# Kernel tuning notes

Hardware: AMD Instinct MI355X
Metric: run time of the kernel (lower is better)

Reference implementation:

```python
import jax, jax.numpy as jnp
from jax import lax
import numpy as np

NPOINT, K, EPS = 2048, 16, 1e-5


def fps(xyz, npoint):
    # Farthest point sampling. Deterministic start index 0 (torch uses randint).
    B, N, _ = xyz.shape
    def step(carry, _):
        distance, far = carry
        centroid = jnp.take_along_axis(xyz, far[:, None, None], axis=1)  # [B,1,3]
        d = jnp.sum((xyz - centroid) ** 2, axis=-1)                      # [B,N]
        distance = jnp.minimum(distance, d)
        return (distance, jnp.argmax(distance, axis=-1)), far
    init = (jnp.full((B, N), 1e10, dtype=xyz.dtype), jnp.zeros((B,), jnp.int32))
    _, cent = lax.scan(step, init, None, length=npoint)  # [npoint, B]
    return jnp.transpose(cent)  # [B, npoint]


def gather(points, idx):
    # points [B,N,C], idx [B,...] -> [B,...,C]
    return jax.vmap(lambda p, i: p[i])(points, idx)


def bn_relu(x, gamma, beta):
    # x [B,S,K,C]; BatchNorm2d training-mode stats over (B,S,K) per channel
    mu = jnp.mean(x, axis=(0, 1, 2), keepdims=True)
    var = jnp.var(x, axis=(0, 1, 2), keepdims=True)
    return jax.nn.relu((x - mu) * lax.rsqrt(var + EPS) * gamma + beta)


def setup_inputs() -> dict:
    key = jax.random.key(0)
    ks = jax.random.split(key, 8)
    B, N, C_in, C_out = 4, 8192, 64, 128
    return {
        'xyz': jax.random.normal(ks[0], (B, N, 3), jnp.float32),
        'feat': jax.random.normal(ks[1], (B, N, C_in), jnp.float32),
        'W1': jax.random.normal(ks[2], (C_in + 3, C_out), jnp.float32) * 0.05,
        'g1': jnp.ones((C_out,), jnp.float32),
        'b1': jnp.zeros((C_out,), jnp.float32),
        'W2': jax.random.normal(ks[3], (C_out, C_out), jnp.float32) * 0.05,
        'g2': jnp.ones((C_out,), jnp.float32),
        'b2': jnp.zeros((C_out,), jnp.float32),
    }


def reference(xyz, feat, W1, g1, b1, W2, g2, b2):
    fps_idx = fps(xyz, NPOINT)
    new_xyz = gather(xyz, fps_idx)                              # [B,S,3]
    # squared distances [B,S,N] via ||a||^2 + ||b||^2 - 2 a.b (avoids [B,S,N,3])
    d = (jnp.sum(new_xyz ** 2, -1)[:, :, None]
         + jnp.sum(xyz ** 2, -1)[:, None, :]
         - 2.0 * jnp.einsum('bsc,bnc->bsn', new_xyz, xyz))
    _, idx = lax.top_k(-d, K)                                   # [B,S,K] smallest dists
    g_xyz = gather(xyz, idx)                                    # [B,S,K,3]
    g_feat = gather(feat, idx)                                  # [B,S,K,C]
    x = jnp.concatenate([g_feat, g_xyz - new_xyz[:, :, None]], axis=-1)
    x = bn_relu(jnp.einsum('bskc,co->bsko', x, W1), g1, b1)     # 1x1 conv == matmul
    x = bn_relu(jnp.einsum('bskc,co->bsko', x, W2), g2, b2)
    new_feat = jnp.max(x, axis=2)                               # max over K -> [B,S,Cout]
    return new_xyz, new_feat
```

## Files before the change

kernel.cpp:

```cpp
#include <hip/hip_runtime.h>
#include <hip/hip_bf16.h>

#define N_PTS 8192
#define N_SAMP 2048
#define KNN_K 16
#define NBATCH 4
#define BN_M (NBATCH * N_SAMP * KNN_K)
#define NROWS (N_SAMP * NBATCH * KNN_K)

typedef float f32x2 __attribute__((ext_vector_type(2)));

template <int CTRL, int RM>
__device__ __forceinline__ unsigned umax_dpp(unsigned v) {
  unsigned o = (unsigned)__builtin_amdgcn_update_dpp((int)v, (int)v, CTRL, RM, 0xF, false);
  return (o > v) ? o : v;
}
template <int CTRL, int RM>
__device__ __forceinline__ unsigned umin_dpp(unsigned v) {
  unsigned o = (unsigned)__builtin_amdgcn_update_dpp((int)v, (int)v, CTRL, RM, 0xF, false);
  return (o < v) ? o : v;
}

__global__ __launch_bounds__(1024) void fps_kernel(const float* __restrict__ xyz,
                                                   int* __restrict__ fps_idx,
                                                   float* __restrict__ new_xyz) {
#pragma clang fp contract(off)
  __shared__ __align__(16) float xyzw[N_PTS * 4];
  __shared__ int samp[N_SAMP];
  __shared__ unsigned redbuf[2][16];
  __shared__ unsigned winmin[2];
  const int b = blockIdx.x;
  const int tid = threadIdx.x;
  const int lane = tid & 63;
  const int wid = tid >> 6;
  const float* base = xyz + (size_t)b * N_PTS * 3;
  for (int i = tid; i < N_PTS * 3; i += 1024) {
    float v = base[i];
    int p = i / 3, c = i - p * 3;
    xyzw[p * 4 + c] = v;
  }
  for (int i = tid; i < N_PTS; i += 1024) xyzw[i * 4 + 3] = 0.f;
  if (tid == 0) { samp[0] = 0; winmin[0] = 0u; winmin[1] = 0xFFFFFFFFu; }
  __syncthreads();

  f32x2 px[4], py[4], pz[4], dmin[4];
#pragma unroll
  for (int j = 0; j < 4; ++j) {
    int p0 = (2 * j) * 1024 + tid, p1 = p0 + 1024;
    const float4 a = *reinterpret_cast<const float4*>(&xyzw[p0 * 4]);
    const float4 c = *reinterpret_cast<const float4*>(&xyzw[p1 * 4]);
    px[j] = f32x2{a.x, c.x};
    py[j] = f32x2{a.y, c.y};
    pz[j] = f32x2{a.z, c.z};
    dmin[j] = f32x2{1e10f, 1e10f};
  }
  unsigned cur = 0;
  for (int it = 1; it < N_SAMP; ++it) {
    const int p = it & 1;
    const float4 c4 = *reinterpret_cast<const float4*>(&xyzw[cur * 4]);
    f32x2 cX = {c4.x, c4.x}, cY = {c4.y, c4.y}, cZ = {c4.z, c4.z};
#pragma unroll
    for (int j = 0; j < 4; ++j) {
      f32x2 dx = px[j] - cX;
      f32x2 dy = py[j] - cY;
      f32x2 dz = pz[j] - cZ;
      f32x2 s01 = dx * dx + dy * dy;
      f32x2 d = s01 + dz * dz;
      dmin[j] = __builtin_elementwise_min(dmin[j], d);
    }
    f32x2 m0 = __builtin_elementwise_max(dmin[0], dmin[1]);
    f32x2 m1 = __builtin_elementwise_max(dmin[2], dmin[3]);
    f32x2 nn = __builtin_elementwise_max(m0, m1);
    const unsigned bd = __float_as_uint(fmaxf(nn.x, nn.y));
    unsigned r = bd;
    r = umax_dpp<0xB1, 0xF>(r);
    r = umax_dpp<0x4E, 0xF>(r);
    r = umax_dpp<0x124, 0xF>(r);
    r = umax_dpp<0x128, 0xF>(r);
    r = umax_dpp<0x142, 0xA>(r);
    r = umax_dpp<0x143, 0xC>(r);
    const unsigned g_wave = (unsigned)__builtin_amdgcn_readlane((int)r, 63);
    if (lane == 0) redbuf[p][wid] = g_wave;
    __syncthreads();
    unsigned g2 = redbuf[p][lane & 15];
    g2 = umax_dpp<0xB1, 0xF>(g2);
    g2 = umax_dpp<0x4E, 0xF>(g2);
    g2 = umax_dpp<0x124, 0xF>(g2);
    g2 = umax_dpp<0x128, 0xF>(g2);
    if (g_wave == g2) {
      unsigned cand = 0xFFFFFFFFu;
#pragma unroll
      for (int j = 3; j >= 0; --j) {
        cand = (__float_as_uint(dmin[j].y) == g2) ? (unsigned)((2 * j + 1) * 1024 + tid) : cand;
        cand = (__float_as_uint(dmin[j].x) == g2) ? (unsigned)((2 * j) * 1024 + tid) : cand;
      }
      cand = umin_dpp<0xB1, 0xF>(cand);
      cand = umin_dpp<0x4E, 0xF>(cand);
      cand = umin_dpp<0x124, 0xF>(cand);
      cand = umin_dpp<0x128, 0xF>(cand);
      cand = umin_dpp<0x142, 0xA>(cand);
      cand = umin_dpp<0x143, 0xC>(cand);
      const unsigned c_wave = (unsigned)__builtin_amdgcn_readlane((int)cand, 63);
      if (lane == 0) atomicMin(&winmin[p], c_wave);
    }
    __syncthreads();
    cur = winmin[p];
    if (tid == 0) { samp[it] = (int)cur; winmin[p ^ 1] = 0xFFFFFFFFu; }
  }
  __syncthreads();
  for (int s = tid; s < N_SAMP; s += 1024) {
    int idx = samp[s];
    fps_idx[b * N_SAMP + s] = idx;
    size_t o = ((size_t)b * N_SAMP + s) * 3;
    new_xyz[o] = xyzw[idx * 4 + 0];
    new_xyz[o + 1] = xyzw[idx * 4 + 1];
    new_xyz[o + 2] = xyzw[idx * 4 + 2];
  }
}

__global__ __launch_bounds__(256) void knn_kernel(const float* __restrict__ xyz,
                                                  const float* __restrict__ new_xyz,
                                                  int* __restrict__ knn_idx) {
  const int wid = threadIdx.x >> 6, lane = threadIdx.x & 63;
  const int q = blockIdx.x * 4 + wid;
  const int b = q >> 11;
  const float* qp = new_xyz + (size_t)q * 3;
  float q0 = qp[0], q1 = qp[1], q2 = qp[2];
  float qn = __fadd_rn(__fadd_rn(__fmul_rn(q0, q0), __fmul_rn(q1, q1)), __fmul_rn(q2, q2));
  const float* pb = xyz + (size_t)b * N_PTS * 3;
  unsigned long long arr[16];
#pragma unroll
  for (int i = 0; i < 16; ++i) arr[i] = ~0ull;
  for (int p = lane; p < N_PTS; p += 64) {
    float p0 = pb[p * 3 + 0], p1 = pb[p * 3 + 1], p2 = pb[p * 3 + 2];
    float pn = __fadd_rn(__fadd_rn(__fmul_rn(p0, p0), __fmul_rn(p1, p1)), __fmul_rn(p2, p2));
    float dt = fmaf(q2, p2, fmaf(q1, p1, __fmul_rn(q0, p0)));
    float d = __fsub_rn(__fadd_rn(qn, pn), __fmul_rn(2.0f, dt));
    unsigned ub = __float_as_uint(d);
    ub ^= (unsigned)((int)ub >> 31) | 0x80000000u;
    unsigned long long key = ((unsigned long long)ub << 32) | (unsigned)p;
    if (key < arr[15]) {
      unsigned long long curk = key;
#pragma unroll
      for (int j = 0; j < 16; ++j) {
        unsigned long long lo = (curk < arr[j]) ? curk : arr[j];
        unsigned long long hi = (curk < arr[j]) ? arr[j] : curk;
        arr[j] = lo; curk = hi;
      }
    }
  }
  for (int r = 0; r < KNN_K; ++r) {
    unsigned long long m = arr[0];
#pragma unroll
    for (int o = 32; o > 0; o >>= 1) {
      unsigned long long other = __shfl_xor(m, o, 64);
      m = (other < m) ? other : m;
    }
    if (arr[0] == m) {
#pragma unroll
      for (int j = 0; j < 15; ++j) arr[j] = arr[j + 1];
      arr[15] = ~0ull;
    }
    if (lane == r) knn_idx[(size_t)q * KNN_K + r] = (int)(m & 0xFFFFFFFFu);
  }
}

__global__ __launch_bounds__(256) void gemm1_kernel(
    const float* __restrict__ xyz, const float* __restrict__ feat,
    const float* __restrict__ W1, const float* __restrict__ new_xyz,
    const int* __restrict__ knn_i, float* __restrict__ y1, float* __restrict__ stats1) {
  __shared__ __align__(16) float At[67 * 128];
  __shared__ __align__(16) float Wq[17 * 128];
  __shared__ float part[4 * 256];
  __shared__ int nb[128];
  const int t = threadIdx.x, blk = blockIdx.x;
  const int row0 = blk * 128;
  if (t < 128) nb[t] = knn_i[row0 + t];
  __syncthreads();
  {
    const int r = t >> 1, q = t & 1;
    const int rg = row0 + r, bs = rg >> 4, b = bs >> 11;
    const float* fr = feat + ((size_t)b * N_PTS + nb[r]) * 64 + q * 32;
#pragma unroll
    for (int i = 0; i < 8; ++i) {
      float4 v = *reinterpret_cast<const float4*>(fr + 4 * i);
      int c = q * 32 + 4 * i;
      At[(c + 0) * 128 + r] = v.x; At[(c + 1) * 128 + r] = v.y;
      At[(c + 2) * 128 + r] = v.z; At[(c + 3) * 128 + r] = v.w;
    }
    if (q == 0) {
      const float* pr = xyz + ((size_t)b * N_PTS + nb[r]) * 3;
      const float* qr = new_xyz + (size_t)bs * 3;
      At[64 * 128 + r] = pr[0] - qr[0];
      At[65 * 128 + r] = pr[1] - qr[1];
      At[66 * 128 + r] = pr[2] - qr[2];
    }
  }
  float acc[8][8];
#pragma unroll
  for (int i = 0; i < 8; ++i)
#pragma unroll
    for (int j = 0; j < 8; ++j) acc[i][j] = 0.f;
  const int ry = t >> 4, cx = t & 15;
  for (int kq = 0; kq < 4; ++kq) {
    const int kbase = kq * 17;
    const int nk = (67 - kbase) < 17 ? (67 - kbase) : 17;
    __syncthreads();
    for (int i = t; i < nk * 32; i += 256)
      reinterpret_cast<float4*>(Wq)[i] =
          reinterpret_cast<const float4*>(W1 + (size_t)kbase * 128)[i];
    __syncthreads();
    for (int kk = 0; kk < nk; ++kk) {
      const float4 a0 = *reinterpret_cast<const float4*>(&At[(kbase + kk) * 128 + ry * 8]);
      const float4 a1 = *reinterpret_cast<const float4*>(&At[(kbase + kk) * 128 + ry * 8 + 4]);
      const float4 w0 = *reinterpret_cast<const float4*>(&Wq[kk * 128 + cx * 8]);
      const float4 w1 = *reinterpret_cast<const float4*>(&Wq[kk * 128 + cx * 8 + 4]);
      const float a[8] = {a0.x, a0.y, a0.z, a0.w, a1.x, a1.y, a1.z, a1.w};
      const float w[8] = {w0.x, w0.y, w0.z, w0.w, w1.x, w1.y, w1.z, w1.w};
#pragma unroll
      for (int i = 0; i < 8; ++i)
#pragma unroll
        for (int j = 0; j < 8; ++j) acc[i][j] = fmaf(a[i], w[j], acc[i][j]);
    }
  }
#pragma unroll
  for (int i = 0; i < 8; ++i) {
    float4 v0 = {acc[i][0], acc[i][1], acc[i][2], acc[i][3]};
    float4 v1 = {acc[i][4], acc[i][5], acc[i][6], acc[i][7]};
    float* dst = y1 + ((size_t)row0 + ry * 8 + i) * 128 + cx * 8;
    *reinterpret_cast<float4*>(dst) = v0;
    *reinterpret_cast<float4*>(dst + 4) = v1;
  }
  float s8[8], q8[8];
#pragma unroll
  for (int j = 0; j < 8; ++j) {
    s8[j] = 0.f; q8[j] = 0.f;
#pragma unroll
    for (int i = 0; i < 8; ++i) { s8[j] += acc[i][j]; q8[j] += acc[i][j] * acc[i][j]; }
  }
#pragma unroll
  for (int j = 0; j < 8; ++j) {
    s8[j] += __shfl_xor(s8[j], 16, 64); q8[j] += __shfl_xor(q8[j], 16, 64);
    s8[j] += __shfl_xor(s8[j], 32, 64); q8[j] += __shfl_xor(q8[j], 32, 64);
  }
  const int w = t >> 6, lane = t & 63;
  if (lane < 16) {
#pragma unroll
    for (int j = 0; j < 8; ++j) {
      part[w * 256 + lane * 8 + j] = s8[j];
      part[w * 256 + 128 + lane * 8 + j] = q8[j];
    }
  }
  __syncthreads();
  {
    int ch = t & 127, which = t >> 7;
    float v = part[0 * 256 + which * 128 + ch] + part[1 * 256 + which * 128 + ch] +
              part[2 * 256 + which * 128 + ch] + part[3 * 256 + which * 128 + ch];
    atomicAdd(&stats1[which * 128 + ch], v);
  }
}

__global__ __launch_bounds__(256) void gemm2_kernel(
    const float* __restrict__ y1, const float* __restrict__ W2,
    const float* __restrict__ stats1, const float* __restrict__ g1v,
    const float* __restrict__ b1v, float* __restrict__ y2, float* __restrict__ stats2) {
  __shared__ __align__(16) float Ah[64 * 128];
  __shared__ __align__(16) float Wq[32 * 128];
  __shared__ float part[4 * 256];
  __shared__ float s1[128], h1[128];
  const int t = threadIdx.x, blk = blockIdx.x;
  const int row0 = blk * 128;
  const float inv_m = 1.0f / (float)BN_M;
  if (t < 128) {
    float m = stats1[t] * inv_m;
    float var = stats1[128 + t] * inv_m - m * m;
    float rs = rsqrtf(var + 1e-5f);
    float sc = rs * g1v[t];
    s1[t] = sc;
    h1[t] = b1v[t] - m * sc;
  }
  float acc[8][8];
#pragma unroll
  for (int i = 0; i < 8; ++i)
#pragma unroll
    for (int j = 0; j < 8; ++j) acc[i][j] = 0.f;
  const int ry = t >> 4, cx = t & 15;
  for (int kh = 0; kh < 2; ++kh) {
    __syncthreads();
    {
      const int r = t >> 1, q = t & 1;
      const float* src = y1 + ((size_t)row0 + r) * 128 + kh * 64 + q * 32;
#pragma unroll
      for (int i = 0; i < 8; ++i) {
        float4 v = *reinterpret_cast<const float4*>(src + 4 * i);
        int c = kh * 64 + q * 32 + 4 * i;
        int cl = c - kh * 64;
        Ah[(cl + 0) * 128 + r] = fmaxf(fmaf(v.x, s1[c + 0], h1[c + 0]), 0.f);
        Ah[(cl + 1) * 128 + r] = fmaxf(fmaf(v.y, s1[c + 1], h1[c + 1]), 0.f);
        Ah[(cl + 2) * 128 + r] = fmaxf(fmaf(v.z, s1[c + 2], h1[c + 2]), 0.f);
        Ah[(cl + 3) * 128 + r] = fmaxf(fmaf(v.w, s1[c + 3], h1[c + 3]), 0.f);
      }
    }
    for (int kq = 0; kq < 2; ++kq) {
      __syncthreads();
      const int kbase = kh * 64 + kq * 32;
      for (int i = t; i < 32 * 32; i += 256)
        reinterpret_cast<float4*>(Wq)[i] =
            reinterpret_cast<const float4*>(W2 + (size_t)kbase * 128)[i];
      __syncthreads();
      for (int kk = 0; kk < 32; ++kk) {
        const int kl = kq * 32 + kk;
        const float4 a0 = *reinterpret_cast<const float4*>(&Ah[kl * 128 + ry * 8]);
        const float4 a1 = *reinterpret_cast<const float4*>(&Ah[kl * 128 + ry * 8 + 4]);
        const float4 w0 = *reinterpret_cast<const float4*>(&Wq[kk * 128 + cx * 8]);
        const float4 w1 = *reinterpret_cast<const float4*>(&Wq[kk * 128 + cx * 8 + 4]);
        const float a[8] = {a0.x, a0.y, a0.z, a0.w, a1.x, a1.y, a1.z, a1.w};
        const float w[8] = {w0.x, w0.y, w0.z, w0.w, w1.x, w1.y, w1.z, w1.w};
#pragma unroll
        for (int i = 0; i < 8; ++i)
#pragma unroll
          for (int j = 0; j < 8; ++j) acc[i][j] = fmaf(a[i], w[j], acc[i][j]);
      }
    }
  }
#pragma unroll
  for (int i = 0; i < 8; ++i) {
    float4 v0 = {acc[i][0], acc[i][1], acc[i][2], acc[i][3]};
    float4 v1 = {acc[i][4], acc[i][5], acc[i][6], acc[i][7]};
    float* dst = y2 + ((size_t)row0 + ry * 8 + i) * 128 + cx * 8;
    *reinterpret_cast<float4*>(dst) = v0;
    *reinterpret_cast<float4*>(dst + 4) = v1;
  }
  float s8[8], q8[8];
#pragma unroll
  for (int j = 0; j < 8; ++j) {
    s8[j] = 0.f; q8[j] = 0.f;
#pragma unroll
    for (int i = 0; i < 8; ++i) { s8[j] += acc[i][j]; q8[j] += acc[i][j] * acc[i][j]; }
  }
#pragma unroll
  for (int j = 0; j < 8; ++j) {
    s8[j] += __shfl_xor(s8[j], 16, 64); q8[j] += __shfl_xor(q8[j], 16, 64);
    s8[j] += __shfl_xor(s8[j], 32, 64); q8[j] += __shfl_xor(q8[j], 32, 64);
  }
  const int w = t >> 6, lane = t & 63;
  if (lane < 16) {
#pragma unroll
    for (int j = 0; j < 8; ++j) {
      part[w * 256 + lane * 8 + j] = s8[j];
      part[w * 256 + 128 + lane * 8 + j] = q8[j];
    }
  }
  __syncthreads();
  {
    int ch = t & 127, which = t >> 7;
    float v = part[0 * 256 + which * 128 + ch] + part[1 * 256 + which * 128 + ch] +
              part[2 * 256 + which * 128 + ch] + part[3 * 256 + which * 128 + ch];
    atomicAdd(&stats2[which * 128 + ch], v);
  }
}

__global__ __launch_bounds__(256) void pool_kernel(
    const float* __restrict__ y2, const float* __restrict__ stats2,
    const float* __restrict__ g2v, const float* __restrict__ b2v,
    float* __restrict__ out_feat) {
  __shared__ float s2[128], h2[128];
  __shared__ float part[4 * 128];
  const int t = threadIdx.x, blk = blockIdx.x;
  const float inv_m = 1.0f / (float)BN_M;
  if (t < 128) {
    float m = stats2[t] * inv_m;
    float var = stats2[128 + t] * inv_m - m * m;
    float rs = rsqrtf(var + 1e-5f);
    float sc = rs * g2v[t];
    s2[t] = sc;
    h2[t] = b2v[t] - m * sc;
  }
  __syncthreads();
  const int c4 = (t & 31) * 4, rg = t >> 5;
  const int lane = t & 63, w = t >> 6;
  for (int s = 0; s < 8; ++s) {
    const int bs = blk * 8 + s;
    float4 m4 = {-1e30f, -1e30f, -1e30f, -1e30f};
#pragma unroll
    for (int rr = 0; rr < 2; ++rr) {
      const int r = bs * 16 + rg * 2 + rr;
      float4 v = *reinterpret_cast<const float4*>(y2 + (size_t)r * 128 + c4);
      float4 z = {fmaxf(fmaf(v.x, s2[c4 + 0], h2[c4 + 0]), 0.f),
                  fmaxf(fmaf(v.y, s2[c4 + 1], h2[c4 + 1]), 0.f),
                  fmaxf(fmaf(v.z, s2[c4 + 2], h2[c4 + 2]), 0.f),
                  fmaxf(fmaf(v.w, s2[c4 + 3], h2[c4 + 3]), 0.f)};
      m4.x = fmaxf(m4.x, z.x); m4.y = fmaxf(m4.y, z.y);
      m4.z = fmaxf(m4.z, z.z); m4.w = fmaxf(m4.w, z.w);
    }
    m4.x = fmaxf(m4.x, __shfl_xor(m4.x, 32, 64));
    m4.y = fmaxf(m4.y, __shfl_xor(m4.y, 32, 64));
    m4.z = fmaxf(m4.z, __shfl_xor(m4.z, 32, 64));
    m4.w = fmaxf(m4.w, __shfl_xor(m4.w, 32, 64));
    if (lane < 32) {
      part[w * 128 + c4 + 0] = m4.x; part[w * 128 + c4 + 1] = m4.y;
      part[w * 128 + c4 + 2] = m4.z; part[w * 128 + c4 + 3] = m4.w;
    }
    __syncthreads();
    if (t < 128) {
      float mm = fmaxf(fmaxf(part[t], part[128 + t]), fmaxf(part[256 + t], part[384 + t]));
      out_feat[(size_t)bs * 128 + t] = mm;
    }
    __syncthreads();
  }
}

extern "C" void kernel_launch(void* const* d_in, const int* in_sizes, int n_in,
                              void* d_out, int out_size, void* d_ws, size_t ws_size,
                              hipStream_t stream) {
  const float* xyz  = (const float*)d_in[0];
  const float* feat = (const float*)d_in[1];
  const float* W1   = (const float*)d_in[2];
  const float* g1   = (const float*)d_in[3];
  const float* b1   = (const float*)d_in[4];
  const float* W2   = (const float*)d_in[5];
  const float* g2   = (const float*)d_in[6];
  const float* b2   = (const float*)d_in[7];
  float* out = (float*)d_out;
  float* new_xyz = out;
  float* out_feat = out + NBATCH * N_SAMP * 3;

  int* fps_i = (int*)d_ws;
  int* knn_i = fps_i + NBATCH * N_SAMP;
  float* stats1 = (float*)(knn_i + NROWS);
  float* stats2 = stats1 + 256;
  float* y1 = stats2 + 256;
  float* y2 = y1 + (size_t)NROWS * 128;

  hipMemsetAsync(stats1, 0, 512 * sizeof(float), stream);
  hipLaunchKernelGGL(fps_kernel, dim3(NBATCH), dim3(1024), 0, stream, xyz, fps_i, new_xyz);
  hipLaunchKernelGGL(knn_kernel, dim3((NBATCH * N_SAMP) / 4), dim3(256), 0, stream,
                     xyz, new_xyz, knn_i);
  hipLaunchKernelGGL(gemm1_kernel, dim3(NROWS / 128), dim3(256), 0, stream,
                     xyz, feat, W1, new_xyz, knn_i, y1, stats1);
  hipLaunchKernelGGL(gemm2_kernel, dim3(NROWS / 128), dim3(256), 0, stream,
                     y1, W2, stats1, g1, b1, y2, stats2);
  hipLaunchKernelGGL(pool_kernel, dim3(NBATCH * N_SAMP / 8), dim3(256), 0, stream,
                     y2, stats2, g2, b2, out_feat);
}
```

Before: 2.323 ms.

## Halve FPS block size and replace wave argmin reduction with per-lane atomicMin

The FPS kernel now runs 512 threads per batch, each holding 16 points instead of 8, so the cross-wave max reduction covers 8 waves instead of 16. The second wave-level DPP min reduction is replaced by each matching lane issuing an LDS atomicMin directly. The winner slot is read at the start of the next iteration and the slot reset is moved into the existing barrier window. Together these cut per-iteration synchronisation and reduction latency in this serial 2048-step loop, at the cost of more per-thread work and register pressure.

```diff
diff --git a/kernel.cpp b/kernel.cpp
--- a/kernel.cpp
+++ b/kernel.cpp
@@ -15,38 +15,33 @@
   unsigned o = (unsigned)__builtin_amdgcn_update_dpp((int)v, (int)v, CTRL, RM, 0xF, false);
   return (o > v) ? o : v;
 }
-template <int CTRL, int RM>
-__device__ __forceinline__ unsigned umin_dpp(unsigned v) {
-  unsigned o = (unsigned)__builtin_amdgcn_update_dpp((int)v, (int)v, CTRL, RM, 0xF, false);
-  return (o < v) ? o : v;
-}
-
-__global__ __launch_bounds__(1024) void fps_kernel(const float* __restrict__ xyz,
-                                                   int* __restrict__ fps_idx,
-                                                   float* __restrict__ new_xyz) {
+
+__global__ __launch_bounds__(512) void fps_kernel(const float* __restrict__ xyz,
+                                                  int* __restrict__ fps_idx,
+                                                  float* __restrict__ new_xyz) {
 #pragma clang fp contract(off)
   __shared__ __align__(16) float xyzw[N_PTS * 4];
   __shared__ int samp[N_SAMP];
-  __shared__ unsigned redbuf[2][16];
-  __shared__ unsigned winmin[2];
+  __shared__ unsigned redbuf[8];
+  __shared__ unsigned winslot[2];
   const int b = blockIdx.x;
   const int tid = threadIdx.x;
   const int lane = tid & 63;
   const int wid = tid >> 6;
   const float* base = xyz + (size_t)b * N_PTS * 3;
-  for (int i = tid; i < N_PTS * 3; i += 1024) {
+  for (int i = tid; i < N_PTS * 3; i += 512) {
     float v = base[i];
     int p = i / 3, c = i - p * 3;
     xyzw[p * 4 + c] = v;
   }
-  for (int i = tid; i < N_PTS; i += 1024) xyzw[i * 4 + 3] = 0.f;
-  if (tid == 0) { samp[0] = 0; winmin[0] = 0u; winmin[1] = 0xFFFFFFFFu; }
-  __syncthreads();
-
-  f32x2 px[4], py[4], pz[4], dmin[4];
-#pragma unroll
-  for (int j = 0; j < 4; ++j) {
-    int p0 = (2 * j) * 1024 + tid, p1 = p0 + 1024;
+  for (int i = tid; i < N_PTS; i += 512) xyzw[i * 4 + 3] = 0.f;
+  if (tid == 0) { winslot[0] = 0u; winslot[1] = 0xFFFFFFFFu; }
+  __syncthreads();
+
+  f32x2 px[8], py[8], pz[8], dmin[8];
+#pragma unroll
+  for (int j = 0; j < 8; ++j) {
+    int p0 = (2 * j) * 512 + tid, p1 = p0 + 512;
     const float4 a = *reinterpret_cast<const float4*>(&xyzw[p0 * 4]);
     const float4 c = *reinterpret_cast<const float4*>(&xyzw[p1 * 4]);
     px[j] = f32x2{a.x, c.x};
@@ -54,23 +49,29 @@
     pz[j] = f32x2{a.z, c.z};
     dmin[j] = f32x2{1e10f, 1e10f};
   }
-  unsigned cur = 0;
   for (int it = 1; it < N_SAMP; ++it) {
     const int p = it & 1;
+    const unsigned cur = winslot[p ^ 1];
+    if (tid == 0) samp[it - 1] = (int)cur;
     const float4 c4 = *reinterpret_cast<const float4*>(&xyzw[cur * 4]);
     f32x2 cX = {c4.x, c4.x}, cY = {c4.y, c4.y}, cZ = {c4.z, c4.z};
 #pragma unroll
-    for (int j = 0; j < 4; ++j) {
+    for (int j = 0; j < 8; ++j) {
       f32x2 dx = px[j] - cX;
       f32x2 dy = py[j] - cY;
       f32x2 dz = pz[j] - cZ;
       f32x2 s01 = dx * dx + dy * dy;
       f32x2 d = s01 + dz * dz;
-      dmin[j] = __builtin_elementwise_min(dmin[j], d);
-    }
-    f32x2 m0 = __builtin_elementwise_max(dmin[0], dmin[1]);
-    f32x2 m1 = __builtin_elementwise_max(dmin[2], dmin[3]);
-    f32x2 nn = __builtin_elementwise_max(m0, m1);
+      dmin[j].x = fminf(dmin[j].x, d.x);
+      dmin[j].y = fminf(dmin[j].y, d.y);
+    }
+    f32x2 m0 = {fmaxf(dmin[0].x, dmin[1].x), fmaxf(dmin[0].y, dmin[1].y)};
+    f32x2 m1 = {fmaxf(dmin[2].x, dmin[3].x), fmaxf(dmin[2].y, dmin[3].y)};
+    f32x2 m2 = {fmaxf(dmin[4].x, dmin[5].x), fmaxf(dmin[4].y, dmin[5].y)};
+    f32x2 m3 = {fmaxf(dmin[6].x, dmin[7].x), fmaxf(dmin[6].y, dmin[7].y)};
+    f32x2 n0 = {fmaxf(m0.x, m1.x), fmaxf(m0.y, m1.y)};
+    f32x2 n1 = {fmaxf(m2.x, m3.x), fmaxf(m2.y, m3.y)};
+    f32x2 nn = {fmaxf(n0.x, n1.x), fmaxf(n0.y, n1.y)};
     const unsigned bd = __float_as_uint(fmaxf(nn.x, nn.y));
     unsigned r = bd;
     r = umax_dpp<0xB1, 0xF>(r);
@@ -79,36 +80,27 @@
     r = umax_dpp<0x128, 0xF>(r);
     r = umax_dpp<0x142, 0xA>(r);
     r = umax_dpp<0x143, 0xC>(r);
-    const unsigned g_wave = (unsigned)__builtin_amdgcn_readlane((int)r, 63);
-    if (lane == 0) redbuf[p][wid] = g_wave;
-    __syncthreads();
-    unsigned g2 = redbuf[p][lane & 15];
-    g2 = umax_dpp<0xB1, 0xF>(g2);
-    g2 = umax_dpp<0x4E, 0xF>(g2);
-    g2 = umax_dpp<0x124, 0xF>(g2);
-    g2 = umax_dpp<0x128, 0xF>(g2);
-    if (g_wave == g2) {
+    if (lane == 63) redbuf[wid] = r;
+    __syncthreads();
+    if (tid == 0) winslot[p ^ 1] = 0xFFFFFFFFu;
+    unsigned g = redbuf[lane & 7];
+    g = umax_dpp<0xB1, 0xF>(g);
+    g = umax_dpp<0x4E, 0xF>(g);
+    g = umax_dpp<0x124, 0xF>(g);
+    if (bd == g) {
       unsigned cand = 0xFFFFFFFFu;
 #pragma unroll
-      for (int j = 3; j >= 0; --j) {
-        cand = (__float_as_uint(dmin[j].y) == g2) ? (unsigned)((2 * j + 1) * 1024 + tid) : cand;
-        cand = (__float_as_uint(dmin[j].x) == g2) ? (unsigned)((2 * j) * 1024 + tid) : cand;
+      for (int j = 7; j >= 0; --j) {
+        if (__float_as_uint(dmin[j].y) == g) cand = (unsigned)((2 * j + 1) * 512 + tid);
+        if (__float_as_uint(dmin[j].x) == g) cand = (unsigned)((2 * j) * 512 + tid);
       }
-      cand = umin_dpp<0xB1, 0xF>(cand);
-      cand = umin_dpp<0x4E, 0xF>(cand);
-      cand = umin_dpp<0x124, 0xF>(cand);
-      cand = umin_dpp<0x128, 0xF>(cand);
-      cand = umin_dpp<0x142, 0xA>(cand);
-      cand = umin_dpp<0x143, 0xC>(cand);
-      const unsigned c_wave = (unsigned)__builtin_amdgcn_readlane((int)cand, 63);
-      if (lane == 0) atomicMin(&winmin[p], c_wave);
-    }
-    __syncthreads();
-    cur = winmin[p];
-    if (tid == 0) { samp[it] = (int)cur; winmin[p ^ 1] = 0xFFFFFFFFu; }
-  }
-  __syncthreads();
-  for (int s = tid; s < N_SAMP; s += 1024) {
+      atomicMin(&winslot[p], cand);
+    }
+    __syncthreads();
+  }
+  if (tid == 0) samp[N_SAMP - 1] = (int)winslot[(N_SAMP - 1) & 1];
+  __syncthreads();
+  for (int s = tid; s < N_SAMP; s += 512) {
     int idx = samp[s];
     fps_idx[b * N_SAMP + s] = idx;
     size_t o = ((size_t)b * N_SAMP + s) * 3;
@@ -433,7 +425,7 @@
   float* y2 = y1 + (size_t)NROWS * 128;
 
   hipMemsetAsync(stats1, 0, 512 * sizeof(float), stream);
-  hipLaunchKernelGGL(fps_kernel, dim3(NBATCH), dim3(1024), 0, stream, xyz, fps_i, new_xyz);
+  hipLaunchKernelGGL(fps_kernel, dim3(NBATCH), dim3(512), 0, stream, xyz, fps_i, new_xyz);
   hipLaunchKernelGGL(knn_kernel, dim3((NBATCH * N_SAMP) / 4), dim3(256), 0, stream,
                      xyz, new_xyz, knn_i);
   hipLaunchKernelGGL(gemm1_kernel, dim3(NROWS / 128), dim3(256), 0, stream,
```

Result: faster. 2.233 ms (-3.9%).
